# Optimization experiments

Hardware: AMD Instinct MI355X
Metric: run time of the kernel (lower is better)

The kernel has to match this reference:

```python
import jax, jax.numpy as jnp
import numpy as np

D_MODEL = 1024
NUM_HEADS = 16
HEAD_DIM = D_MODEL // NUM_HEADS
B, L = 2, 2048


def setup_inputs() -> dict:
    key = jax.random.key(0)
    ks = jax.random.split(key, 9)
    s = 0.02
    return {
        "query": jax.random.normal(ks[0], (B, L, D_MODEL), dtype=jnp.float32),
        "key": jax.random.normal(ks[1], (B, L, D_MODEL), dtype=jnp.float32),
        "value": jax.random.normal(ks[2], (B, L, D_MODEL), dtype=jnp.float32),
        "mask": jax.random.randint(ks[3], (B, L), 0, 2, dtype=jnp.int32),
        "Wq": jax.random.normal(ks[4], (D_MODEL, D_MODEL), dtype=jnp.float32) * s,
        "Wk": jax.random.normal(ks[5], (D_MODEL, D_MODEL), dtype=jnp.float32) * s,
        "Wv": jax.random.normal(ks[6], (D_MODEL, D_MODEL), dtype=jnp.float32) * s,
        "Wo": jax.random.normal(ks[7], (D_MODEL, D_MODEL), dtype=jnp.float32) * s,
        "bo": jnp.zeros((D_MODEL,), dtype=jnp.float32),
    }


def _split_heads(x):
    # (B, L, d_model) -> (B, H, L, head_dim)
    b, l, _ = x.shape
    return x.reshape(b, l, NUM_HEADS, HEAD_DIM).transpose(0, 2, 1, 3)


def reference(query, key, value, mask, Wq, Wk, Wv, Wo, bo):
    # nn.Linear(bias=False): x @ W.T
    q = _split_heads(query @ Wq.T)   # (B, H, L, hd)
    k = _split_heads(key @ Wk.T)
    v = _split_heads(value @ Wv.T)

    scores = jnp.einsum("bhqd,bhkd->bhqk", q, k) / jnp.sqrt(jnp.float32(HEAD_DIM))
    # padding mask over keys: (B, L) -> (B, 1, 1, L); 0 = pad -> -inf
    keep = (mask[:, None, None, :] != 0)
    scores = jnp.where(keep, scores, -jnp.inf)

    attn = jax.nn.softmax(scores, axis=-1)
    # original zeroes NaN rows (fully-masked query rows)
    attn = jnp.where(jnp.isnan(attn), jnp.zeros_like(attn), attn)
    # dropout is identity in eval/reference mode

    ctx = jnp.einsum("bhqk,bhkd->bhqd", attn, v)           # (B, H, L, hd)
    ctx = ctx.transpose(0, 2, 1, 3).reshape(B, L, D_MODEL)  # combine heads
    return ctx @ Wo.T + bo
```

## Files before the change

kernel.cpp:

```cpp
#include <hip/hip_runtime.h>

typedef unsigned short u16;
typedef __bf16 bf16x8 __attribute__((ext_vector_type(8)));
typedef __bf16 bf16x4 __attribute__((ext_vector_type(4)));
typedef float floatx4 __attribute__((ext_vector_type(4)));
typedef u16 u16x4 __attribute__((ext_vector_type(4)));
typedef unsigned uint32x2 __attribute__((ext_vector_type(2)));
typedef unsigned uint32x4 __attribute__((ext_vector_type(4)));

#define MEG ((size_t)(1u << 20))

__device__ __forceinline__ u16 f2bf(float f) {
  unsigned int u = __float_as_uint(f);
  u += 0x7fffu + ((u >> 16) & 1u);
  return (u16)(u >> 16);
}

__device__ __forceinline__ unsigned cvt_pk_bf16(float lo, float hi) {
  unsigned r;
  asm("v_cvt_pk_bf16_f32 %0, %1, %2" : "=v"(r) : "v"(lo), "v"(hi));
  return r;
}

__device__ __forceinline__ void load_lds16(const u16* g, u16* l) {
  __builtin_amdgcn_global_load_lds((const __attribute__((address_space(1))) unsigned int*)g,
                                   (__attribute__((address_space(3))) unsigned int*)l,
                                   16, 0, 0);
}

__global__ __launch_bounds__(256) void cvt7(
    const float* __restrict__ s0, const float* __restrict__ s1,
    const float* __restrict__ s2, const float* __restrict__ s3,
    const float* __restrict__ s4, const float* __restrict__ s5,
    const float* __restrict__ s6, u16* __restrict__ dst)
{
  size_t e = ((size_t)blockIdx.x * 256 + threadIdx.x) * 16;
  unsigned m = (unsigned)(e >> 20);
  const float* s; size_t off;
  if (m < 4)       { s = s0; off = e; }
  else if (m < 8)  { s = s1; off = e - 4 * MEG; }
  else if (m < 12) { s = s2; off = e - 8 * MEG; }
  else if (m < 13) { s = s3; off = e - 12 * MEG; }
  else if (m < 14) { s = s4; off = e - 13 * MEG; }
  else if (m < 15) { s = s5; off = e - 14 * MEG; }
  else             { s = s6; off = e - 15 * MEG; }
  float4 f[4];
#pragma unroll
  for (int t = 0; t < 4; ++t)
    f[t] = *reinterpret_cast<const float4*>(s + off + t * 4);
#pragma unroll
  for (int t = 0; t < 4; ++t) {
    u16x4 o;
    o.x = f2bf(f[t].x); o.y = f2bf(f[t].y); o.z = f2bf(f[t].z); o.w = f2bf(f[t].w);
    *reinterpret_cast<u16x4*>(dst + e + t * 4) = o;
  }
}

__global__ __launch_bounds__(256) void gemm_proj(
    const u16* __restrict__ Abase, const u16* __restrict__ Bbase,
    u16* __restrict__ Cbase, u16* __restrict__ VtB,
    int K, long zA, long zB, long zC)
{
  __shared__ __align__(16) u16 As[128 * 64];
  __shared__ __align__(16) u16 Bs[128 * 64];
  const int tid = threadIdx.x;
  const int w = tid >> 6, ln = tid & 63;
  const int lm = ln & 15, lq = ln >> 4;
  const int wm = w >> 1, wn = w & 1;
  const long m0 = (long)blockIdx.x * 128, n0 = (long)blockIdx.y * 128;
  const u16* A = Abase + (size_t)blockIdx.z * (size_t)zA;
  const u16* B = Bbase + (size_t)blockIdx.z * (size_t)zB;

  const int r0 = tid >> 3;
  const int kc = (tid & 7) ^ (r0 & 7);
  const u16* gA = A + (m0 + r0) * (long)K + kc * 8;
  const u16* gB = B + (n0 + r0) * (long)K + kc * 8;
  const long rstep = 32L * K;

  const int sl0 = (lq ^ (lm & 7)) * 8;
  const int sl1 = ((4 + lq) ^ (lm & 7)) * 8;
  const u16* ab0 = &As[(wm * 64 + lm) * 64 + sl0];
  const u16* ab1 = &As[(wm * 64 + lm) * 64 + sl1];
  const u16* bb0 = &Bs[(wn * 64 + lm) * 64 + sl0];
  const u16* bb1 = &Bs[(wn * 64 + lm) * 64 + sl1];

  const floatx4 z4 = {0.f, 0.f, 0.f, 0.f};
  floatx4 acc[4][4];
#pragma unroll
  for (int i = 0; i < 4; ++i)
#pragma unroll
    for (int j = 0; j < 4; ++j) acc[i][j] = z4;

  for (int k0 = 0; k0 < K; k0 += 64) {
#pragma unroll
    for (int t = 0; t < 4; ++t) {
      load_lds16(gA + t * rstep, &As[(t * 256 + w * 64) * 8]);
      load_lds16(gB + t * rstep, &Bs[(t * 256 + w * 64) * 8]);
    }
    gA += 64; gB += 64;
    __syncthreads();
    bf16x8 af[4][2], bfr[4][2];
#pragma unroll
    for (int i = 0; i < 4; ++i) {
      af[i][0] = *reinterpret_cast<const bf16x8*>(ab0 + i * 1024);
      af[i][1] = *reinterpret_cast<const bf16x8*>(ab1 + i * 1024);
    }
#pragma unroll
    for (int j = 0; j < 4; ++j) {
      bfr[j][0] = *reinterpret_cast<const bf16x8*>(bb0 + j * 1024);
      bfr[j][1] = *reinterpret_cast<const bf16x8*>(bb1 + j * 1024);
    }
#pragma unroll
    for (int i = 0; i < 4; ++i)
#pragma unroll
      for (int j = 0; j < 4; ++j) {
        acc[i][j] = __builtin_amdgcn_mfma_f32_16x16x32_bf16(af[i][0], bfr[j][0], acc[i][j], 0, 0, 0);
        acc[i][j] = __builtin_amdgcn_mfma_f32_16x16x32_bf16(af[i][1], bfr[j][1], acc[i][j], 0, 0, 0);
      }
    __syncthreads();
  }

  if (blockIdx.z == 2) {
#pragma unroll
    for (int i = 0; i < 4; ++i) {
      long row = m0 + wm * 64 + i * 16 + lq * 4;
      int bq = (int)(row >> 11);
      int l  = (int)(row & 2047);
#pragma unroll
      for (int j = 0; j < 4; ++j) {
        long col = n0 + wn * 64 + j * 16 + lm;
        int hh = (int)(col >> 6), dd = (int)(col & 63);
        u16x4 o;
        o.x = f2bf(acc[i][j][0]); o.y = f2bf(acc[i][j][1]);
        o.z = f2bf(acc[i][j][2]); o.w = f2bf(acc[i][j][3]);
        *reinterpret_cast<u16x4*>(&VtB[((size_t)(bq * 16 + hh)) * 131072 +
                                       (size_t)dd * 2048 + l]) = o;
      }
    }
    return;
  }

#pragma unroll
  for (int i = 0; i < 4; ++i) {
    long row = m0 + wm * 64 + i * 16 + lq * 4;
#pragma unroll
    for (int j = 0; j < 4; ++j) {
      long col = n0 + wn * 64 + j * 16 + lm;
#pragma unroll
      for (int r = 0; r < 4; ++r) {
        size_t idx = (size_t)(row + r) * 1024 + (size_t)col;
        (Cbase + (size_t)blockIdx.z * (size_t)zC)[idx] = f2bf(acc[i][j][r]);
      }
    }
  }
}

__global__ __launch_bounds__(256) void gemm_out_fused(
    const u16* __restrict__ OpA, const u16* __restrict__ OpB,
    const float* __restrict__ psA, const float* __restrict__ psB,
    const u16* __restrict__ Wo, const float* __restrict__ bias,
    float* __restrict__ Cout)
{
  __shared__ __align__(16) u16 As[64 * 64];
  __shared__ __align__(16) u16 Bs[128 * 64];
  const int tid = threadIdx.x;
  const int w = tid >> 6, ln = tid & 63;
  const int lm = ln & 15, lq = ln >> 4;
  const int wm = w >> 1, wn = w & 1;
  const long m0 = (long)blockIdx.x * 64, n0 = (long)blockIdx.y * 128;

  const int r0 = tid >> 3;
  const int kc = (tid & 7) ^ (r0 & 7);
  const u16* gB = Wo + (n0 + r0) * 1024 + kc * 8;
  const long rstep = 32L * 1024;

  const int sl0 = (lq ^ (lm & 7)) * 8;
  const int sl1 = ((4 + lq) ^ (lm & 7)) * 8;
  const u16* ab0 = &As[(wm * 32 + lm) * 64 + sl0];
  const u16* ab1 = &As[(wm * 32 + lm) * 64 + sl1];
  const u16* bb0 = &Bs[(wn * 64 + lm) * 64 + sl0];
  const u16* bb1 = &Bs[(wn * 64 + lm) * 64 + sl1];

  int rowg[2]; int qlb[2];
#pragma unroll
  for (int t = 0; t < 2; ++t) {
    rowg[t] = (int)m0 + r0 + t * 32;
    int b = rowg[t] >> 11, l = rowg[t] & 2047;
    qlb[t] = (b << 4) * 2048 + l;
  }

  const floatx4 z4 = {0.f, 0.f, 0.f, 0.f};
  floatx4 acc[2][4];
#pragma unroll
  for (int i = 0; i < 2; ++i)
#pragma unroll
    for (int j = 0; j < 4; ++j) acc[i][j] = z4;

  for (int k0 = 0; k0 < 1024; k0 += 64) {
#pragma unroll
    for (int t = 0; t < 4; ++t)
      load_lds16(gB + t * rstep, &Bs[(t * 256 + w * 64) * 8]);
    gB += 64;
    const int h = k0 >> 6;
#pragma unroll
    for (int t = 0; t < 2; ++t) {
      int ql = qlb[t] + h * 2048;
      float s = psA[ql] + psB[ql];
      float inv = (s > 0.f) ? __builtin_amdgcn_rcpf(s) : 0.f;
      size_t idx = (size_t)rowg[t] * 1024 + k0 + kc * 8;
      uint4 ua = *reinterpret_cast<const uint4*>(OpA + idx);
      uint4 ub = *reinterpret_cast<const uint4*>(OpB + idx);
      uint4 uo;
      const unsigned* pa = reinterpret_cast<const unsigned*>(&ua);
      const unsigned* pb = reinterpret_cast<const unsigned*>(&ub);
      unsigned* po = reinterpret_cast<unsigned*>(&uo);
#pragma unroll
      for (int i = 0; i < 4; ++i) {
        float alo = __uint_as_float(pa[i] << 16);
        float ahi = __uint_as_float(pa[i] & 0xFFFF0000u);
        float blo = __uint_as_float(pb[i] << 16);
        float bhi = __uint_as_float(pb[i] & 0xFFFF0000u);
        float olo = (alo + blo) * inv;
        float ohi = (ahi + bhi) * inv;
        po[i] = (unsigned)f2bf(olo) | ((unsigned)f2bf(ohi) << 16);
      }
      *reinterpret_cast<uint4*>(&As[(size_t)(t * 256 + tid) * 8]) = uo;
    }
    __syncthreads();
    bf16x8 af[2][2], bfr[4][2];
#pragma unroll
    for (int i = 0; i < 2; ++i) {
      af[i][0] = *reinterpret_cast<const bf16x8*>(ab0 + i * 1024);
      af[i][1] = *reinterpret_cast<const bf16x8*>(ab1 + i * 1024);
    }
#pragma unroll
    for (int j = 0; j < 4; ++j) {
      bfr[j][0] = *reinterpret_cast<const bf16x8*>(bb0 + j * 1024);
      bfr[j][1] = *reinterpret_cast<const bf16x8*>(bb1 + j * 1024);
    }
#pragma unroll
    for (int i = 0; i < 2; ++i)
#pragma unroll
      for (int j = 0; j < 4; ++j) {
        acc[i][j] = __builtin_amdgcn_mfma_f32_16x16x32_bf16(af[i][0], bfr[j][0], acc[i][j], 0, 0, 0);
        acc[i][j] = __builtin_amdgcn_mfma_f32_16x16x32_bf16(af[i][1], bfr[j][1], acc[i][j], 0, 0, 0);
      }
    __syncthreads();
  }

#pragma unroll
  for (int i = 0; i < 2; ++i) {
    long row = m0 + wm * 32 + i * 16 + lq * 4;
#pragma unroll
    for (int j = 0; j < 4; ++j) {
      long col = n0 + wn * 64 + j * 16 + lm;
      float bv = bias[col];
#pragma unroll
      for (int r = 0; r < 4; ++r)
        Cout[(size_t)(row + r) * 1024 + (size_t)col] = acc[i][j][r] + bv;
    }
  }
}

__global__ __launch_bounds__(256, 4) void attn_kernel(
    const u16* __restrict__ Qp, const u16* __restrict__ Kp,
    const u16* __restrict__ Vt, const int* __restrict__ mask,
    u16* __restrict__ OpBase, float* __restrict__ psAB)
{
  __shared__ __align__(16) u16 Ks[2 * 64 * 64];
  __shared__ __align__(16) u16 Vts[2 * 64 * 64];
  __shared__ __align__(16) float mball[1024];

  const int tid = threadIdx.x;
  const int w = tid >> 6, ln = tid & 63;
  const int lm = ln & 15, lq = ln >> 4;

  const int lid = blockIdx.x + (blockIdx.y << 4) + (blockIdx.z << 9);
  const int xcd = lid & 7, slot = lid >> 3;
  const int group = (xcd << 3) + (slot >> 4);
  const int qt = slot & 15;
  const int kz = group & 1;
  const int bh = group >> 1, b = bh >> 4, h = bh & 15;
  const int q0 = qt * 128;

  const u16* Qh = Qp + (size_t)b * 2048 * 1024 + h * 64;
  const u16* Kh = Kp + (size_t)b * 2048 * 1024 + (size_t)kz * 1024 * 1024 + h * 64;
  const u16* Vth = Vt + (size_t)bh * 64 * 2048 + kz * 1024;
  u16* Op = OpBase + (size_t)kz * 8 * MEG;
  float* psZ = psAB + (size_t)kz * 65536;

  const int* mrowp = mask + b * 2048 + kz * 1024;
#pragma unroll
  for (int t = 0; t < 4; ++t) {
    int i = t * 256 + tid;
    mball[i] = (mrowp[i] != 0) ? 0.f : -__builtin_inff();
  }

  bf16x8 qf[2][2];
#pragma unroll
  for (int m = 0; m < 2; ++m) {
    int qrow = q0 + w * 32 + m * 16 + lm;
    qf[m][0] = *reinterpret_cast<const bf16x8*>(Qh + (size_t)qrow * 1024 + lq * 8);
    qf[m][1] = *reinterpret_cast<const bf16x8*>(Qh + (size_t)qrow * 1024 + 32 + lq * 8);
  }

  const int sl0 = (lq ^ (lm & 7)) * 8;
  const int sl1 = ((4 + lq) ^ (lm & 7)) * 8;
  const u16* kb0 = &Ks[lm * 64 + sl0];
  const u16* kb1 = &Ks[lm * 64 + sl1];
  const u16* vb0 = &Vts[lm * 64 + sl0];
  const u16* vb1 = &Vts[lm * 64 + sl1];
  const float* mbi = mball + lq * 4;

  const int r0 = tid >> 3;
  const int kc = (tid & 7) ^ (r0 & 7);
  const u16* gK0 = Kh + (size_t)r0 * 1024 + kc * 8;
  const u16* gK1 = gK0 + 32 * 1024;
  const u16* gV0 = Vth + (size_t)r0 * 2048 + kc * 8;
  const u16* gV1 = gV0 + 32 * 2048;

  const floatx4 z4 = {0.f, 0.f, 0.f, 0.f};
  floatx4 O[2][4];
#pragma unroll
  for (int m = 0; m < 2; ++m)
#pragma unroll
    for (int j = 0; j < 4; ++j) O[m][j] = z4;
  float psum[2] = {0.f, 0.f};
  const float SCL = 0.18033688011112042f;

  load_lds16(gK0, &Ks[(w * 64) * 8]);
  load_lds16(gK1, &Ks[(256 + w * 64) * 8]);
  load_lds16(gV0, &Vts[(w * 64) * 8]);
  load_lds16(gV1, &Vts[(256 + w * 64) * 8]);
  gK0 += 64 * 1024; gK1 += 64 * 1024; gV0 += 64; gV1 += 64;
  __syncthreads();

  for (int it = 0; it < 16; ++it) {
    const int cur = it & 1;
    if (it < 15) {
      const int nx = (cur ^ 1) * 4096;
      load_lds16(gK0, &Ks[nx + (w * 64) * 8]);
      load_lds16(gK1, &Ks[nx + (256 + w * 64) * 8]);
      load_lds16(gV0, &Vts[nx + (w * 64) * 8]);
      load_lds16(gV1, &Vts[nx + (256 + w * 64) * 8]);
      gK0 += 64 * 1024; gK1 += 64 * 1024; gV0 += 64; gV1 += 64;
    }
    const int bofs = cur * 4096;

    float4 mb4[4];
#pragma unroll
    for (int n = 0; n < 4; ++n)
      mb4[n] = *reinterpret_cast<const float4*>(mbi + n * 16);
    mbi += 64;

#pragma unroll
    for (int h2 = 0; h2 < 2; ++h2) {
      floatx4 S[2][2];
      {
        bf16x8 k00 = *reinterpret_cast<const bf16x8*>(kb0 + bofs + (2 * h2) * 1024);
        bf16x8 k01 = *reinterpret_cast<const bf16x8*>(kb1 + bofs + (2 * h2) * 1024);
        bf16x8 k10 = *reinterpret_cast<const bf16x8*>(kb0 + bofs + (2 * h2 + 1) * 1024);
        bf16x8 k11 = *reinterpret_cast<const bf16x8*>(kb1 + bofs + (2 * h2 + 1) * 1024);
        __builtin_amdgcn_s_setprio(1);
#pragma unroll
        for (int m = 0; m < 2; ++m) {
          S[m][0] = __builtin_amdgcn_mfma_f32_16x16x32_bf16(k00, qf[m][0], z4, 0, 0, 0);
          S[m][0] = __builtin_amdgcn_mfma_f32_16x16x32_bf16(k01, qf[m][1], S[m][0], 0, 0, 0);
          S[m][1] = __builtin_amdgcn_mfma_f32_16x16x32_bf16(k10, qf[m][0], z4, 0, 0, 0);
          S[m][1] = __builtin_amdgcn_mfma_f32_16x16x32_bf16(k11, qf[m][1], S[m][1], 0, 0, 0);
        }
        __builtin_amdgcn_s_setprio(0);
      }

      float4 mbA = mb4[2 * h2];
      float4 mbB = mb4[2 * h2 + 1];
      bf16x8 pf[2];
#pragma unroll
      for (int m = 0; m < 2; ++m) {
        float a0 = __builtin_amdgcn_exp2f(fmaf(S[m][0][0], SCL, mbA.x));
        float a1 = __builtin_amdgcn_exp2f(fmaf(S[m][0][1], SCL, mbA.y));
        float a2 = __builtin_amdgcn_exp2f(fmaf(S[m][0][2], SCL, mbA.z));
        float a3 = __builtin_amdgcn_exp2f(fmaf(S[m][0][3], SCL, mbA.w));
        psum[m] += (a0 + a1) + (a2 + a3);
        unsigned c00 = cvt_pk_bf16(a0, a1);
        unsigned c01 = cvt_pk_bf16(a2, a3);
        float b0 = __builtin_amdgcn_exp2f(fmaf(S[m][1][0], SCL, mbB.x));
        float b1 = __builtin_amdgcn_exp2f(fmaf(S[m][1][1], SCL, mbB.y));
        float b2 = __builtin_amdgcn_exp2f(fmaf(S[m][1][2], SCL, mbB.z));
        float b3 = __builtin_amdgcn_exp2f(fmaf(S[m][1][3], SCL, mbB.w));
        psum[m] += (b0 + b1) + (b2 + b3);
        unsigned c10 = cvt_pk_bf16(b0, b1);
        unsigned c11 = cvt_pk_bf16(b2, b3);

        uint32x2 t1a = __builtin_amdgcn_permlane32_swap(c00, c10, false, false);
        uint32x2 t2a = __builtin_amdgcn_permlane16_swap(t1a.x, t1a.y, false, false);
        uint32x2 t1b = __builtin_amdgcn_permlane32_swap(c01, c11, false, false);
        uint32x2 t2b = __builtin_amdgcn_permlane16_swap(t1b.x, t1b.y, false, false);
        uint32x4 wv = {t2a.x, t2b.x, t2a.y, t2b.y};
        pf[m] = __builtin_bit_cast(bf16x8, wv);
      }

      const u16* vb = (h2 ? vb1 : vb0) + bofs;
      __builtin_amdgcn_s_setprio(1);
#pragma unroll
      for (int j = 0; j < 4; ++j) {
        bf16x8 vfj = *reinterpret_cast<const bf16x8*>(vb + j * 1024);
        O[0][j] = __builtin_amdgcn_mfma_f32_16x16x32_bf16(pf[0], vfj, O[0][j], 0, 0, 0);
        O[1][j] = __builtin_amdgcn_mfma_f32_16x16x32_bf16(pf[1], vfj, O[1][j], 0, 0, 0);
      }
      __builtin_amdgcn_s_setprio(0);
    }
    __syncthreads();
  }

#pragma unroll
  for (int m = 0; m < 2; ++m) {
    float s = psum[m];
    s += __shfl_xor(s, 16, 64);
    s += __shfl_xor(s, 32, 64);
    int prow = q0 + w * 32 + m * 16 + lm;
    if (lq == 0) psZ[bh * 2048 + prow] = s;
#pragma unroll
    for (int r = 0; r < 4; ++r) {
      int row = q0 + w * 32 + m * 16 + lq * 4 + r;
      size_t base = ((size_t)b * 2048 + row) * 1024 + h * 64 + lm;
#pragma unroll
      for (int j = 0; j < 4; ++j)
        Op[base + j * 16] = f2bf(O[m][j][r]);
    }
  }
}

extern "C" void kernel_launch(void* const* d_in, const int* in_sizes, int n_in,
                              void* d_out, int out_size, void* d_ws, size_t ws_size,
                              hipStream_t stream) {
  const float* q  = (const float*)d_in[0];
  const float* k  = (const float*)d_in[1];
  const float* v  = (const float*)d_in[2];
  const int*   mk = (const int*)  d_in[3];
  const float* wq = (const float*)d_in[4];
  const float* wk = (const float*)d_in[5];
  const float* wv = (const float*)d_in[6];
  const float* wo = (const float*)d_in[7];
  const float* bo = (const float*)d_in[8];

  u16* ws16 = (u16*)d_ws;
  u16* Xq  = ws16;
  u16* Wq  = ws16 + 12 * MEG;
  u16* Wo  = ws16 + 15 * MEG;
  u16* Qp  = ws16 + 16 * MEG;
  u16* Kp  = ws16 + 20 * MEG;
  u16* Vt  = ws16 + 24 * MEG;
  u16* OpA = ws16;
  u16* OpB = ws16 + 8 * MEG;
  float* psAB = (float*)(ws16 + 12 * MEG);

  cvt7<<<dim3(4096), dim3(256), 0, stream>>>(q, k, v, wq, wk, wv, wo, ws16);

  gemm_proj<<<dim3(32, 8, 3), dim3(256), 0, stream>>>(
      Xq, Wq, Qp, Vt, 1024, (long)(4 * MEG), (long)MEG, (long)(4 * MEG));

  attn_kernel<<<dim3(16, 32, 2), dim3(256), 0, stream>>>(Qp, Kp, Vt, mk, OpA, psAB);

  gemm_out_fused<<<dim3(64, 8), dim3(256), 0, stream>>>(
      OpA, OpB, psAB, psAB + 65536, Wo, bo, (float*)d_out);
}
```

Measured before the change: 219.2 us.

## Fuse fp32-to-bf16 conversion of inputs and weights into projection GEMM

Removes the separate conversion pass over the Q/K/V activations and the Wq/Wk/Wv weights. The projection GEMM now loads fp32 directly from global memory, converts to bf16 in registers and stores into LDS. Only Wo is still converted by a small standalone kernel. This saves writing and re-reading about 30 MB of bf16 intermediates and one launch. In exchange the GEMM loses the async global-to-LDS path, reads twice the bytes per tile, and re-converts each operand tile once per block that reuses it.

Result: slower. 240.2 us (+9.6%).

```diff
diff --git a/kernel.cpp b/kernel.cpp
--- a/kernel.cpp
+++ b/kernel.cpp
@@ -28,26 +28,14 @@
                                    16, 0, 0);
 }
 
-__global__ __launch_bounds__(256) void cvt7(
-    const float* __restrict__ s0, const float* __restrict__ s1,
-    const float* __restrict__ s2, const float* __restrict__ s3,
-    const float* __restrict__ s4, const float* __restrict__ s5,
-    const float* __restrict__ s6, u16* __restrict__ dst)
+__global__ __launch_bounds__(256) void cvt_wo(
+    const float* __restrict__ s, u16* __restrict__ dst)
 {
   size_t e = ((size_t)blockIdx.x * 256 + threadIdx.x) * 16;
-  unsigned m = (unsigned)(e >> 20);
-  const float* s; size_t off;
-  if (m < 4)       { s = s0; off = e; }
-  else if (m < 8)  { s = s1; off = e - 4 * MEG; }
-  else if (m < 12) { s = s2; off = e - 8 * MEG; }
-  else if (m < 13) { s = s3; off = e - 12 * MEG; }
-  else if (m < 14) { s = s4; off = e - 13 * MEG; }
-  else if (m < 15) { s = s5; off = e - 14 * MEG; }
-  else             { s = s6; off = e - 15 * MEG; }
   float4 f[4];
 #pragma unroll
   for (int t = 0; t < 4; ++t)
-    f[t] = *reinterpret_cast<const float4*>(s + off + t * 4);
+    f[t] = *reinterpret_cast<const float4*>(s + e + t * 4);
 #pragma unroll
   for (int t = 0; t < 4; ++t) {
     u16x4 o;
@@ -57,9 +45,10 @@
 }
 
 __global__ __launch_bounds__(256) void gemm_proj(
-    const u16* __restrict__ Abase, const u16* __restrict__ Bbase,
-    u16* __restrict__ Cbase, u16* __restrict__ VtB,
-    int K, long zA, long zB, long zC)
+    const float* __restrict__ Aq, const float* __restrict__ Ak,
+    const float* __restrict__ Av, const float* __restrict__ Bq,
+    const float* __restrict__ Bk, const float* __restrict__ Bv,
+    u16* __restrict__ Qp, u16* __restrict__ Kp, u16* __restrict__ VtB)
 {
   __shared__ __align__(16) u16 As[128 * 64];
   __shared__ __align__(16) u16 Bs[128 * 64];
@@ -68,14 +57,15 @@
   const int lm = ln & 15, lq = ln >> 4;
   const int wm = w >> 1, wn = w & 1;
   const long m0 = (long)blockIdx.x * 128, n0 = (long)blockIdx.y * 128;
-  const u16* A = Abase + (size_t)blockIdx.z * (size_t)zA;
-  const u16* B = Bbase + (size_t)blockIdx.z * (size_t)zB;
+  const int z = blockIdx.z;
+  const float* Af = (z == 0) ? Aq : (z == 1) ? Ak : Av;
+  const float* Bf = (z == 0) ? Bq : (z == 1) ? Bk : Bv;
 
   const int r0 = tid >> 3;
   const int kc = (tid & 7) ^ (r0 & 7);
-  const u16* gA = A + (m0 + r0) * (long)K + kc * 8;
-  const u16* gB = B + (n0 + r0) * (long)K + kc * 8;
-  const long rstep = 32L * K;
+  const float* gA = Af + (m0 + r0) * 1024 + kc * 8;
+  const float* gB = Bf + (n0 + r0) * 1024 + kc * 8;
+  const long rstep = 32L * 1024;
 
   const int sl0 = (lq ^ (lm & 7)) * 8;
   const int sl1 = ((4 + lq) ^ (lm & 7)) * 8;
@@ -91,11 +81,20 @@
 #pragma unroll
     for (int j = 0; j < 4; ++j) acc[i][j] = z4;
 
-  for (int k0 = 0; k0 < K; k0 += 64) {
+  for (int k0 = 0; k0 < 1024; k0 += 64) {
 #pragma unroll
     for (int t = 0; t < 4; ++t) {
-      load_lds16(gA + t * rstep, &As[(t * 256 + w * 64) * 8]);
-      load_lds16(gB + t * rstep, &Bs[(t * 256 + w * 64) * 8]);
+      float4 a0 = *reinterpret_cast<const float4*>(gA + t * rstep);
+      float4 a1 = *reinterpret_cast<const float4*>(gA + t * rstep + 4);
+      float4 b0 = *reinterpret_cast<const float4*>(gB + t * rstep);
+      float4 b1 = *reinterpret_cast<const float4*>(gB + t * rstep + 4);
+      uint4 ua, ub;
+      ua.x = cvt_pk_bf16(a0.x, a0.y); ua.y = cvt_pk_bf16(a0.z, a0.w);
+      ua.z = cvt_pk_bf16(a1.x, a1.y); ua.w = cvt_pk_bf16(a1.z, a1.w);
+      ub.x = cvt_pk_bf16(b0.x, b0.y); ub.y = cvt_pk_bf16(b0.z, b0.w);
+      ub.z = cvt_pk_bf16(b1.x, b1.y); ub.w = cvt_pk_bf16(b1.z, b1.w);
+      *reinterpret_cast<uint4*>(&As[(size_t)(t * 256 + tid) * 8]) = ua;
+      *reinterpret_cast<uint4*>(&Bs[(size_t)(t * 256 + tid) * 8]) = ub;
     }
     gA += 64; gB += 64;
     __syncthreads();
@@ -120,7 +119,7 @@
     __syncthreads();
   }
 
-  if (blockIdx.z == 2) {
+  if (z == 2) {
 #pragma unroll
     for (int i = 0; i < 4; ++i) {
       long row = m0 + wm * 64 + i * 16 + lq * 4;
@@ -140,6 +139,7 @@
     return;
   }
 
+  u16* C = (z == 0) ? Qp : Kp;
 #pragma unroll
   for (int i = 0; i < 4; ++i) {
     long row = m0 + wm * 64 + i * 16 + lq * 4;
@@ -149,7 +149,7 @@
 #pragma unroll
       for (int r = 0; r < 4; ++r) {
         size_t idx = (size_t)(row + r) * 1024 + (size_t)col;
-        (Cbase + (size_t)blockIdx.z * (size_t)zC)[idx] = f2bf(acc[i][j][r]);
+        C[idx] = f2bf(acc[i][j][r]);
       }
     }
   }
@@ -445,9 +445,7 @@
   const float* bo = (const float*)d_in[8];
 
   u16* ws16 = (u16*)d_ws;
-  u16* Xq  = ws16;
-  u16* Wq  = ws16 + 12 * MEG;
-  u16* Wo  = ws16 + 15 * MEG;
+  u16* WoB = ws16 + 15 * MEG;
   u16* Qp  = ws16 + 16 * MEG;
   u16* Kp  = ws16 + 20 * MEG;
   u16* Vt  = ws16 + 24 * MEG;
@@ -455,13 +453,13 @@
   u16* OpB = ws16 + 8 * MEG;
   float* psAB = (float*)(ws16 + 12 * MEG);
 
-  cvt7<<<dim3(4096), dim3(256), 0, stream>>>(q, k, v, wq, wk, wv, wo, ws16);
+  cvt_wo<<<dim3(256), dim3(256), 0, stream>>>(wo, WoB);
 
   gemm_proj<<<dim3(32, 8, 3), dim3(256), 0, stream>>>(
-      Xq, Wq, Qp, Vt, 1024, (long)(4 * MEG), (long)MEG, (long)(4 * MEG));
+      q, k, v, wq, wk, wv, Qp, Kp, Vt);
 
   attn_kernel<<<dim3(16, 32, 2), dim3(256), 0, stream>>>(Qp, Kp, Vt, mk, OpA, psAB);
 
   gemm_out_fused<<<dim3(64, 8), dim3(256), 0, stream>>>(
-      OpA, OpB, psAB, psAB + 65536, Wo, bo, (float*)d_out);
-}
+      OpA, OpB, psAB, psAB + 65536, WoB, bo, (float*)d_out);
+}
```
